# Kernel optimization log

Hardware: AMD Instinct MI355X
Metric: run time of the kernel (lower is better)

The kernel has to match this reference:

```python
import jax, jax.numpy as jnp
import numpy as np

B, S, D, MAX_LEN = 8, 2048, 512, 2048
NEG_INF = jnp.float32(-jnp.inf)


def setup_inputs() -> dict:
    key = jax.random.key(0)
    ks = jax.random.split(key, 10)
    s = 1.0 / np.sqrt(D)
    inp = {
        "x": jax.random.normal(ks[0], (B, S, D), dtype=jnp.float32),
        "pos_table": jax.random.normal(ks[1], (MAX_LEN, D), dtype=jnp.float32) * 0.02,
        "Wq": jax.random.normal(ks[2], (D, D), dtype=jnp.float32) * s,
        "bq": jnp.zeros((D,), dtype=jnp.float32),
        "Wk": jax.random.normal(ks[3], (D, D), dtype=jnp.float32) * s,
        "bk": jnp.zeros((D,), dtype=jnp.float32),
        "Wv": jax.random.normal(ks[4], (D, D), dtype=jnp.float32) * s,
        "bv": jnp.zeros((D,), dtype=jnp.float32),
        "Wd": jax.random.normal(ks[5], (D, D), dtype=jnp.float32) * s,
        "bd": jnp.zeros((D,), dtype=jnp.float32),
    }
    return inp


def reference(x, pos_table, Wq, bq, Wk, bk, Wv, bv, Wd, bd):
    # add learned positional embeddings (add_pos=True path): arange over seq dim
    x = x + pos_table[:x.shape[-2]]  # [B,S,D]
    # torch nn.Linear: y = x @ W.T + b
    q = jnp.einsum("bsd,ed->bse", x, Wq) + bq
    k = jnp.einsum("bsd,ed->bse", x, Wk) + bk
    v = jnp.einsum("bsd,ed->bse", x, Wv) + bv
    v = jnp.where(jnp.isnan(v), 0.0, v)  # nan_to_num(nan=0)
    scale = 1.0 / jnp.sqrt(jnp.float32(D))
    scores = jnp.einsum("bqd,bkd->bqk", q, k) * scale  # [B,S,S]
    scores = jnp.where(jnp.isnan(scores), NEG_INF, scores)  # nan_to_num(nan=-inf)
    attn = jax.nn.softmax(scores, axis=2)
    y = jnp.einsum("bqk,bkd->bqd", attn, v)
    return jnp.einsum("bsd,ed->bse", y, Wd) + bd
```

## Files before the change

kernel.cpp:

```cpp
#include <hip/hip_runtime.h>
#include <stdint.h>

typedef __bf16 bf16x8 __attribute__((ext_vector_type(8)));
typedef float f32x4 __attribute__((ext_vector_type(4)));

static constexpr float QK_SCALE = 0.044194173824159216f;

__device__ __forceinline__ uint16_t f2bf(float f) {
    uint32_t x = __builtin_bit_cast(uint32_t, f);
    x += 0x7FFFu + ((x >> 16) & 1u);
    return (uint16_t)(x >> 16);
}

__device__ __forceinline__ void cp16(const uint16_t* g, uint16_t* l) {
    __builtin_amdgcn_global_load_lds(
        (__attribute__((address_space(1))) void*)(uint16_t*)g,
        (__attribute__((address_space(3))) void*)l,
        16, 0, 0);
}

template <int MODE>
__global__ __launch_bounds__(256, 3) void gemm_nt(
    const uint16_t* __restrict__ A, const uint16_t* __restrict__ Bm,
    void* __restrict__ C0, void* __restrict__ C1, void* __restrict__ C2,
    const float* __restrict__ bias0, const float* __restrict__ bias1,
    const float* __restrict__ bias2,
    float scale, int K, int ldc, long bsA, long bsB, long bsC)
{
    __shared__ __align__(16) uint16_t SH[2][8192];

    const int t  = threadIdx.x;
    const int bn = blockIdx.x, bm = blockIdx.y, bz = blockIdx.z;
    const int wave = t >> 6, lane = t & 63;
    const int wm = (wave >> 1) * 64, wn = (wave & 1) * 64;
    const int lm = lane & 15, lq = lane >> 4;
    const int sw = lq ^ ((lm >> 1) & 3);

    const uint16_t* Ab = A  + (long)bz * bsA + (long)bm * 128 * K;
    const uint16_t* Bb = Bm + (long)bz * bsB + (long)bn * 128 * K;

    long goff[2]; int loff[2];
#pragma unroll
    for (int j = 0; j < 2; ++j) {
        const int s  = j * 256 + t;
        const int r  = s >> 2;
        const int cs = s & 3;
        const int cg = cs ^ ((r >> 1) & 3);
        goff[j] = (long)r * K + cg * 8;
        loff[j] = s * 8;
    }

    f32x4 acc[4][4] = {};

#pragma unroll
    for (int j = 0; j < 2; ++j) {
        cp16(Ab + goff[j], SH[0] + loff[j]);
        cp16(Bb + goff[j], SH[0] + 4096 + loff[j]);
    }

    int cur = 0;
    for (int k0 = 0; k0 < K; k0 += 32) {
        __syncthreads();
        if (k0 + 32 < K) {
            const int nxt = cur ^ 1;
#pragma unroll
            for (int j = 0; j < 2; ++j) {
                cp16(Ab + goff[j] + k0 + 32, SH[nxt] + loff[j]);
                cp16(Bb + goff[j] + k0 + 32, SH[nxt] + 4096 + loff[j]);
            }
        }

        bf16x8 af[4], bfr[4];
#pragma unroll
        for (int i = 0; i < 4; ++i)
            af[i] = *(const bf16x8*)&SH[cur][((wm + i * 16 + lm) * 4 + sw) * 8];
#pragma unroll
        for (int j = 0; j < 4; ++j)
            bfr[j] = *(const bf16x8*)&SH[cur][4096 + ((wn + j * 16 + lm) * 4 + sw) * 8];
#pragma unroll
        for (int i = 0; i < 4; ++i)
#pragma unroll
            for (int j = 0; j < 4; ++j)
                acc[i][j] = __builtin_amdgcn_mfma_f32_16x16x32_bf16(
                    af[i], bfr[j], acc[i][j], 0, 0, 0);
        cur ^= 1;
    }

    const int mbase = bm * 128 + wm + lq * 4;
    const int nbase = bn * 128 + wn + lm;
#pragma unroll
    for (int i = 0; i < 4; ++i) {
#pragma unroll
        for (int j = 0; j < 4; ++j) {
            const int n = nbase + j * 16;
#pragma unroll
            for (int r = 0; r < 4; ++r) {
                const int m = mbase + i * 16 + r;
                const float v = acc[i][j][r] * scale;
                if (MODE == 0) {
                    ((uint16_t*)C0)[(long)bz * bsC + (long)m * ldc + n] = f2bf(v);
                } else if (MODE == 2) {
                    ((float*)C0)[(long)m * ldc + n] = v + bias0[n];
                } else {
                    const int sec = n >> 9;
                    const int nn  = n & 511;
                    if (sec == 0) {
                        ((uint16_t*)C0)[(long)m * 512 + nn] = f2bf(v + bias0[nn]);
                    } else if (sec == 1) {
                        ((uint16_t*)C1)[(long)m * 512 + nn] = f2bf(v + bias1[nn]);
                    } else {
                        const int bb = m >> 11, ss = m & 2047;
                        ((uint16_t*)C2)[((long)bb * 512 + nn) * 2048 + ss] =
                            f2bf(v + bias2[nn]);
                    }
                }
            }
        }
    }
}

__global__ __launch_bounds__(256) void prep_x(const float* __restrict__ x,
                                              const float* __restrict__ pos,
                                              uint16_t* __restrict__ xb)
{
    const long i8 = ((long)blockIdx.x * 256 + threadIdx.x) * 8;
    const long p8 = i8 & ((1l << 20) - 1);
    const float4* xv = (const float4*)(x + i8);
    const float4* pv = (const float4*)(pos + p8);
    const float4 a0 = xv[0], a1 = xv[1];
    const float4 b0 = pv[0], b1 = pv[1];
    uint16_t o[8];
    o[0] = f2bf(a0.x + b0.x); o[1] = f2bf(a0.y + b0.y);
    o[2] = f2bf(a0.z + b0.z); o[3] = f2bf(a0.w + b0.w);
    o[4] = f2bf(a1.x + b1.x); o[5] = f2bf(a1.y + b1.y);
    o[6] = f2bf(a1.z + b1.z); o[7] = f2bf(a1.w + b1.w);
    *(uint4*)(xb + i8) = *(uint4*)o;
}

__global__ __launch_bounds__(256) void prep_w(
    const float* __restrict__ Wq, const float* __restrict__ Wk,
    const float* __restrict__ Wv, const float* __restrict__ Wd,
    uint16_t* __restrict__ wqkv, uint16_t* __restrict__ wd)
{
    const long f = ((long)blockIdx.x * 256 + threadIdx.x) * 8;
    const int  w = (int)(f >> 18);
    const long off = f & 262143;
    const float* src = (w == 0) ? Wq : (w == 1) ? Wk : (w == 2) ? Wv : Wd;
    uint16_t* dst = (w < 3) ? (wqkv + (long)w * 262144 + off) : (wd + off);
    const float4* s4 = (const float4*)(src + off);
    const float4 a = s4[0], b = s4[1];
    uint16_t o[8];
    o[0] = f2bf(a.x); o[1] = f2bf(a.y); o[2] = f2bf(a.z); o[3] = f2bf(a.w);
    o[4] = f2bf(b.x); o[5] = f2bf(b.y); o[6] = f2bf(b.z); o[7] = f2bf(b.w);
    *(uint4*)dst = *(uint4*)o;
}

__global__ __launch_bounds__(256) void softmax_rows(uint16_t* __restrict__ P)
{
    uint16_t* p = P + (long)blockIdx.x * 2048;
    const int t = threadIdx.x;
    const int lane = t & 63, wave = t >> 6;

    uint4 raw = *(const uint4*)(p + t * 8);
    uint32_t u[4] = {raw.x, raw.y, raw.z, raw.w};
    float x[8];
#pragma unroll
    for (int i = 0; i < 4; ++i) {
        x[2 * i]     = __builtin_bit_cast(float, u[i] << 16);
        x[2 * i + 1] = __builtin_bit_cast(float, u[i] & 0xFFFF0000u);
    }
    float mx = x[0];
#pragma unroll
    for (int i = 1; i < 8; ++i) mx = fmaxf(mx, x[i]);
#pragma unroll
    for (int off = 32; off; off >>= 1) mx = fmaxf(mx, __shfl_xor(mx, off));
    __shared__ float sm[4], ss[4];
    if (lane == 0) sm[wave] = mx;
    __syncthreads();
    mx = fmaxf(fmaxf(sm[0], sm[1]), fmaxf(sm[2], sm[3]));

    float sum = 0.f;
#pragma unroll
    for (int i = 0; i < 8; ++i) { x[i] = __expf(x[i] - mx); sum += x[i]; }
#pragma unroll
    for (int off = 32; off; off >>= 1) sum += __shfl_xor(sum, off);
    if (lane == 0) ss[wave] = sum;
    __syncthreads();
    const float inv = 1.f / (ss[0] + ss[1] + ss[2] + ss[3]);

#pragma unroll
    for (int i = 0; i < 4; ++i) {
        const uint32_t lo = f2bf(x[2 * i] * inv);
        const uint32_t hi = f2bf(x[2 * i + 1] * inv);
        u[i] = lo | (hi << 16);
    }
    *(uint4*)(p + t * 8) = make_uint4(u[0], u[1], u[2], u[3]);
}

extern "C" void kernel_launch(void* const* d_in, const int* in_sizes, int n_in,
                              void* d_out, int out_size, void* d_ws, size_t ws_size,
                              hipStream_t stream)
{
    const float* x   = (const float*)d_in[0];
    const float* pos = (const float*)d_in[1];
    const float* Wq  = (const float*)d_in[2];
    const float* bq  = (const float*)d_in[3];
    const float* Wk  = (const float*)d_in[4];
    const float* bk  = (const float*)d_in[5];
    const float* Wv  = (const float*)d_in[6];
    const float* bv  = (const float*)d_in[7];
    const float* Wd  = (const float*)d_in[8];
    const float* bd  = (const float*)d_in[9];
    float* out = (float*)d_out;

    char* ws = (char*)d_ws;
    uint16_t* xb   = (uint16_t*)(ws);
    uint16_t* wqkv = (uint16_t*)(ws + 16777216);
    uint16_t* wd   = (uint16_t*)(ws + 18350080);
    uint16_t* Qb   = (uint16_t*)(ws + 18874368);
    uint16_t* Kb   = (uint16_t*)(ws + 35651584);
    uint16_t* Vt   = (uint16_t*)(ws + 52428800);
    uint16_t* Pb   = (uint16_t*)(ws + 69206016);
    uint16_t* yb   = (uint16_t*)(ws + 136314880);

    prep_x<<<4096, 256, 0, stream>>>(x, pos, xb);
    prep_w<<<512, 256, 0, stream>>>(Wq, Wk, Wv, Wd, wqkv, wd);

    gemm_nt<3><<<dim3(12, 128, 1), 256, 0, stream>>>(
        xb, wqkv, Qb, Kb, Vt, bq, bk, bv, 1.0f, 512, 512, 0, 0, 0);

    gemm_nt<0><<<dim3(16, 16, 8), 256, 0, stream>>>(
        Qb, Kb, Pb, nullptr, nullptr, nullptr, nullptr, nullptr,
        QK_SCALE, 512, 2048, (long)2048 * 512, (long)2048 * 512,
        (long)2048 * 2048);

    softmax_rows<<<16384, 256, 0, stream>>>(Pb);

    gemm_nt<0><<<dim3(4, 16, 8), 256, 0, stream>>>(
        Pb, Vt, yb, nullptr, nullptr, nullptr, nullptr, nullptr,
        1.0f, 2048, 512, (long)2048 * 2048, (long)512 * 2048,
        (long)2048 * 512);

    gemm_nt<2><<<dim3(4, 128, 1), 256, 0, stream>>>(
        yb, wd, out, nullptr, nullptr, bd, nullptr, nullptr,
        1.0f, 512, 512, 0, 0, 0);
}
```

Before: 314.6 us.

## Deepen GEMM LDS pipeline to four stages and vectorize epilogue stores

Replaces the double-buffered LDS pipeline in gemm_nt with a four-buffer, three-ahead prefetch ring that waits with explicit s_waitcnt vmcnt plus s_barrier. The wrap-around loads past the last K block are harmless redundant fetches. MFMA operands are swapped so each lane holds four consecutive N columns, which lets the epilogue issue packed uint2/float4 stores and vector bias loads instead of scalar writes. LDS per block doubles and the occupancy hint drops from 3 to 2 blocks, trading occupancy for more memory-latency hiding.

```diff
diff --git a/kernel.cpp b/kernel.cpp
--- a/kernel.cpp
+++ b/kernel.cpp
@@ -20,14 +20,14 @@
 }
 
 template <int MODE>
-__global__ __launch_bounds__(256, 3) void gemm_nt(
+__global__ __launch_bounds__(256, 2) void gemm_nt(
     const uint16_t* __restrict__ A, const uint16_t* __restrict__ Bm,
     void* __restrict__ C0, void* __restrict__ C1, void* __restrict__ C2,
     const float* __restrict__ bias0, const float* __restrict__ bias1,
     const float* __restrict__ bias2,
     float scale, int K, int ldc, long bsA, long bsB, long bsC)
 {
-    __shared__ __align__(16) uint16_t SH[2][8192];
+    __shared__ __align__(16) uint16_t SH[4][8192];
 
     const int t  = threadIdx.x;
     const int bn = blockIdx.x, bm = blockIdx.y, bz = blockIdx.z;
@@ -50,69 +50,92 @@
         loff[j] = s * 8;
     }
 
+    const int KI = K >> 5;
+
+#pragma unroll
+    for (int st = 0; st < 3; ++st)
+#pragma unroll
+        for (int j = 0; j < 2; ++j) {
+            cp16(Ab + goff[j] + st * 32, SH[st] + loff[j]);
+            cp16(Bb + goff[j] + st * 32, SH[st] + 4096 + loff[j]);
+        }
+
     f32x4 acc[4][4] = {};
 
-#pragma unroll
-    for (int j = 0; j < 2; ++j) {
-        cp16(Ab + goff[j], SH[0] + loff[j]);
-        cp16(Bb + goff[j], SH[0] + 4096 + loff[j]);
-    }
-
-    int cur = 0;
-    for (int k0 = 0; k0 < K; k0 += 32) {
-        __syncthreads();
-        if (k0 + 32 < K) {
-            const int nxt = cur ^ 1;
-#pragma unroll
-            for (int j = 0; j < 2; ++j) {
-                cp16(Ab + goff[j] + k0 + 32, SH[nxt] + loff[j]);
-                cp16(Bb + goff[j] + k0 + 32, SH[nxt] + 4096 + loff[j]);
-            }
+    for (int k = 0; k < KI; ++k) {
+        asm volatile("s_waitcnt vmcnt(8) lgkmcnt(0)\n\ts_barrier" ::: "memory");
+
+        int kp = k + 3; if (kp >= KI) kp -= KI;
+        uint16_t* dst = SH[(k + 3) & 3];
+        const long ko = (long)kp * 32;
+#pragma unroll
+        for (int j = 0; j < 2; ++j) {
+            cp16(Ab + goff[j] + ko, dst + loff[j]);
+            cp16(Bb + goff[j] + ko, dst + 4096 + loff[j]);
         }
 
+        const uint16_t* buf = SH[k & 3];
         bf16x8 af[4], bfr[4];
 #pragma unroll
         for (int i = 0; i < 4; ++i)
-            af[i] = *(const bf16x8*)&SH[cur][((wm + i * 16 + lm) * 4 + sw) * 8];
-#pragma unroll
-        for (int j = 0; j < 4; ++j)
-            bfr[j] = *(const bf16x8*)&SH[cur][4096 + ((wn + j * 16 + lm) * 4 + sw) * 8];
+            af[i]  = *(const bf16x8*)&buf[((wm + i * 16 + lm) * 4 + sw) * 8];
+#pragma unroll
+        for (int i = 0; i < 4; ++i)
+            bfr[i] = *(const bf16x8*)&buf[4096 + ((wn + i * 16 + lm) * 4 + sw) * 8];
 #pragma unroll
         for (int i = 0; i < 4; ++i)
 #pragma unroll
             for (int j = 0; j < 4; ++j)
                 acc[i][j] = __builtin_amdgcn_mfma_f32_16x16x32_bf16(
-                    af[i], bfr[j], acc[i][j], 0, 0, 0);
-        cur ^= 1;
-    }
-
-    const int mbase = bm * 128 + wm + lq * 4;
-    const int nbase = bn * 128 + wn + lm;
+                    bfr[i], af[j], acc[i][j], 0, 0, 0);
+    }
+
+    const int mb = bm * 128 + wm + lm;
+    const int nb = bn * 128 + wn + lq * 4;
 #pragma unroll
     for (int i = 0; i < 4; ++i) {
-#pragma unroll
-        for (int j = 0; j < 4; ++j) {
-            const int n = nbase + j * 16;
-#pragma unroll
-            for (int r = 0; r < 4; ++r) {
-                const int m = mbase + i * 16 + r;
-                const float v = acc[i][j][r] * scale;
-                if (MODE == 0) {
-                    ((uint16_t*)C0)[(long)bz * bsC + (long)m * ldc + n] = f2bf(v);
-                } else if (MODE == 2) {
-                    ((float*)C0)[(long)m * ldc + n] = v + bias0[n];
+        const int n = nb + i * 16;
+        if (MODE == 0) {
+#pragma unroll
+            for (int j = 0; j < 4; ++j) {
+                const int m = mb + j * 16;
+                const uint32_t lo = (uint32_t)f2bf(acc[i][j][0] * scale) |
+                                    ((uint32_t)f2bf(acc[i][j][1] * scale) << 16);
+                const uint32_t hi = (uint32_t)f2bf(acc[i][j][2] * scale) |
+                                    ((uint32_t)f2bf(acc[i][j][3] * scale) << 16);
+                *(uint2*)&((uint16_t*)C0)[(long)bz * bsC + (long)m * ldc + n] =
+                    make_uint2(lo, hi);
+            }
+        } else if (MODE == 2) {
+            const float4 b4 = *(const float4*)&bias0[n];
+#pragma unroll
+            for (int j = 0; j < 4; ++j) {
+                const int m = mb + j * 16;
+                *(float4*)&((float*)C0)[(long)m * ldc + n] = make_float4(
+                    acc[i][j][0] + b4.x, acc[i][j][1] + b4.y,
+                    acc[i][j][2] + b4.z, acc[i][j][3] + b4.w);
+            }
+        } else {
+            const int sec = n >> 9, nn = n & 511;
+            const float* bp = sec == 0 ? bias0 : (sec == 1 ? bias1 : bias2);
+            const float4 b4 = *(const float4*)&bp[nn];
+#pragma unroll
+            for (int j = 0; j < 4; ++j) {
+                const int m = mb + j * 16;
+                if (sec < 2) {
+                    uint16_t* Cq = (uint16_t*)(sec == 0 ? C0 : C1);
+                    const uint32_t lo = (uint32_t)f2bf(acc[i][j][0] + b4.x) |
+                                        ((uint32_t)f2bf(acc[i][j][1] + b4.y) << 16);
+                    const uint32_t hi = (uint32_t)f2bf(acc[i][j][2] + b4.z) |
+                                        ((uint32_t)f2bf(acc[i][j][3] + b4.w) << 16);
+                    *(uint2*)&Cq[(long)m * 512 + nn] = make_uint2(lo, hi);
                 } else {
-                    const int sec = n >> 9;
-                    const int nn  = n & 511;
-                    if (sec == 0) {
-                        ((uint16_t*)C0)[(long)m * 512 + nn] = f2bf(v + bias0[nn]);
-                    } else if (sec == 1) {
-                        ((uint16_t*)C1)[(long)m * 512 + nn] = f2bf(v + bias1[nn]);
-                    } else {
-                        const int bb = m >> 11, ss = m & 2047;
-                        ((uint16_t*)C2)[((long)bb * 512 + nn) * 2048 + ss] =
-                            f2bf(v + bias2[nn]);
-                    }
+                    const int bb = m >> 11, ss = m & 2047;
+                    uint16_t* vt = (uint16_t*)C2 + ((long)bb * 512 + nn) * 2048 + ss;
+                    vt[0]        = f2bf(acc[i][j][0] + b4.x);
+                    vt[2048]     = f2bf(acc[i][j][1] + b4.y);
+                    vt[2 * 2048] = f2bf(acc[i][j][2] + b4.z);
+                    vt[3 * 2048] = f2bf(acc[i][j][3] + b4.w);
                 }
             }
         }
```

Measured after the change: 300.9 us. 4.4% less time.
